# Kernel optimization log

Hardware: AMD Instinct MI355X
Metric: run time of the kernel (lower is better)

Reference implementation:

```python
import jax, jax.numpy as jnp
import numpy as np

EPS = 1e-5

def _ln(x, g, b):
    m = jnp.mean(x, axis=-1, keepdims=True)
    v = jnp.var(x, axis=-1, keepdims=True)
    return (x - m) * jax.lax.rsqrt(v + EPS) * g + b

def setup_inputs() -> dict:
    key = jax.random.key(0)
    ks = jax.random.split(key, 8)
    B, N, C, H = 2, 2048, 128, 8
    hid = 768
    s = lambda k, shp, fan: jax.random.normal(k, shp, jnp.float32) * (1.0 / np.sqrt(fan))
    return {
        "x1": jax.random.normal(ks[0], (B, N, C), jnp.float32),
        "x2": jax.random.normal(ks[1], (B, N, C), jnp.float32),
        "x3": jax.random.normal(ks[2], (B, N, C), jnp.float32),
        "ln1_g": jnp.ones((3, C), jnp.float32),
        "ln1_b": jnp.zeros((3, C), jnp.float32),
        "qkv_w": s(ks[3], (3, C, 3 * C), C),      # [branch, in, out]; torch Linear weight transposed
        "proj_w": s(ks[4], (3, C, C), C),
        "proj_b": jnp.zeros((3, C), jnp.float32),
        "ln2_g": jnp.ones((3 * C,), jnp.float32),
        "ln2_b": jnp.zeros((3 * C,), jnp.float32),
        "fc1_w": s(ks[5], (3 * C, hid), 3 * C),
        "fc1_b": jnp.zeros((hid,), jnp.float32),
        "fc2_w": s(ks[6], (hid, 3 * C), hid),
        "fc2_b": jnp.zeros((3 * C,), jnp.float32),
    }

def _branch(x, g, b, w_qkv, w_p, b_p, num_heads=8):
    B, N, C = x.shape
    hd = C // num_heads
    scale = hd ** -0.5
    xn = _ln(x, g, b)
    qkv = (xn @ w_qkv).reshape(B, N, 3, num_heads, hd)
    qkv = jnp.transpose(qkv, (2, 0, 3, 1, 4))  # [3,B,H,N,hd]
    q, k, v = qkv[0], qkv[1], qkv[2]
    attn = jax.nn.softmax(jnp.einsum('bhnd,bhmd->bhnm', q, k) * scale, axis=-1)
    o = jnp.einsum('bhnm,bhmd->bhnd', attn, v)
    o = jnp.transpose(o, (0, 2, 1, 3)).reshape(B, N, C)
    return x + (o @ w_p + b_p)

def reference(x1, x2, x3, ln1_g, ln1_b, qkv_w, proj_w, proj_b,
              ln2_g, ln2_b, fc1_w, fc1_b, fc2_w, fc2_b):
    xs = jnp.stack([x1, x2, x3])  # [3,B,N,C]
    xs = jax.vmap(_branch)(xs, ln1_g, ln1_b, qkv_w, proj_w, proj_b)
    B, N, C = x1.shape
    xc = jnp.transpose(xs, (1, 2, 0, 3)).reshape(B, N, 3 * C)  # concat(x1,x2,x3) on features
    h = jax.nn.gelu(_ln(xc, ln2_g, ln2_b) @ fc1_w + fc1_b, approximate=False)
    xc = xc + (h @ fc2_w + fc2_b)
    return xc[:, :, :C], xc[:, :, C:2 * C], xc[:, :, 2 * C:]
```

## Files before the change

### kernel.cpp

```cpp
#include <hip/hip_runtime.h>
#include <hip/hip_bf16.h>

typedef __hip_bfloat16 bf16;


static __device__ __forceinline__ float b2f(bf16 h) { return __bfloat162float(h); }
static __device__ __forceinline__ bf16 f2b(float f) { return __float2bfloat16(f); }
static __device__ __forceinline__ unsigned short f2bu(float f) {
    bf16 h = f2b(f);
    return *reinterpret_cast<unsigned short*>(&h);
}

typedef __attribute__((ext_vector_type(8))) short short8;
typedef __attribute__((ext_vector_type(4))) short short4v;
typedef __attribute__((ext_vector_type(16))) float f32x16;
typedef __attribute__((ext_vector_type(2))) int int2v;

#define QSCALE 0.36067376022224085f

static __device__ __forceinline__ float xhalf(float x, int hi) {
    auto r = __builtin_amdgcn_permlane32_swap(__float_as_int(x), __float_as_int(x), false, false);
    return __int_as_float(hi ? r[0] : r[1]);
}

__global__ __launch_bounds__(256) void k_wt_all(const float* __restrict__ qkv_w, const float* __restrict__ proj_w,
                                                const float* __restrict__ fc1_w, const float* __restrict__ fc2_w,
                                                bf16* __restrict__ wtq, bf16* __restrict__ wtp,
                                                bf16* __restrict__ wt1, bf16* __restrict__ wt2) {
    int idx = blockIdx.x * 256 + threadIdx.x;
    if (idx < 147456) {
        int b = idx / 49152, i2 = idx % 49152;
        int n = i2 >> 7, k = i2 & 127;
        wtq[idx] = f2b(qkv_w[b * 49152 + k * 384 + n]);
    } else if (idx < 196608) {
        int j = idx - 147456;
        int b = j / 16384, i2 = j % 16384;
        int n = i2 >> 7, k = i2 & 127;
        wtp[j] = f2b(proj_w[b * 16384 + k * 128 + n]);
    } else if (idx < 491520) {
        int j = idx - 196608;
        int n = j / 384, k = j - n * 384;
        wt1[j] = f2b(fc1_w[k * 768 + n]);
    } else {
        int j = idx - 491520;
        int n = j / 768, k = j - n * 768;
        wt2[j] = f2b(fc2_w[k * 384 + n]);
    }
}

__device__ __forceinline__ f32x16 gemm_tile(const short* __restrict__ A, const short* __restrict__ W,
                                            int K, int rowbase, int colbase,
                                            short* als, short* wls) {
    int tid = threadIdx.x;
    int wid = tid >> 6, lane = tid & 63;
    int hi = lane >> 5, l31 = lane & 31;
    int wm = wid >> 1, wn = wid & 1;
    int sr = tid >> 3, skb = tid & 7;
    f32x16 acc;
#pragma unroll
    for (int i = 0; i < 16; ++i) acc[i] = 0.f;
    for (int k0 = 0; k0 < K; k0 += 64) {
        __syncthreads();
#pragma unroll
        for (int pass = 0; pass < 2; ++pass) {
            int r = sr + pass * 32;
            short8 av = *(const short8*)&A[(size_t)(rowbase + r) * K + k0 + skb * 8];
            *(short8*)&als[r * 64 + ((skb ^ (r & 7)) * 8)] = av;
            short8 wv = *(const short8*)&W[(size_t)(colbase + r) * K + k0 + skb * 8];
            *(short8*)&wls[r * 64 + ((skb ^ (r & 7)) * 8)] = wv;
        }
        __syncthreads();
#pragma unroll
        for (int ks = 0; ks < 4; ++ks) {
            int ra = wm * 32 + l31;
            int rb = wn * 32 + l31;
            int kb = ks * 2 + hi;
            short8 af = *(const short8*)&als[ra * 64 + ((kb ^ (ra & 7)) * 8)];
            short8 bf = *(const short8*)&wls[rb * 64 + ((kb ^ (rb & 7)) * 8)];
            acc = __builtin_amdgcn_mfma_f32_32x32x16_bf16(af, bf, acc, 0, 0, 0);
        }
    }
    return acc;
}

__global__ __launch_bounds__(256) void k_ln1(const float* __restrict__ x1, const float* __restrict__ x2,
                                             const float* __restrict__ x3, const float* __restrict__ g,
                                             const float* __restrict__ b, bf16* __restrict__ xn) {
    int tid = threadIdx.x;
    int wave = tid >> 6, lane = tid & 63;
    int grow = blockIdx.x * 4 + wave;
    int branch = grow >> 12;
    const float* xp = (branch == 0) ? x1 : (branch == 1 ? x2 : x3);
    const float* row = xp + (size_t)(grow & 4095) * 128;
    float2 a = *reinterpret_cast<const float2*>(&row[2 * lane]);
    float s = a.x + a.y, sq = a.x * a.x + a.y * a.y;
#pragma unroll
    for (int off = 32; off >= 1; off >>= 1) { s += __shfl_xor(s, off); sq += __shfl_xor(sq, off); }
    float mean = s * (1.f / 128.f);
    float var = sq * (1.f / 128.f) - mean * mean;
    float rstd = rsqrtf(var + 1e-5f);
    float2 gv = *reinterpret_cast<const float2*>(&g[branch * 128 + 2 * lane]);
    float2 bv = *reinterpret_cast<const float2*>(&b[branch * 128 + 2 * lane]);
    bf16* orow = xn + (size_t)grow * 128;
    orow[2 * lane] = f2b((a.x - mean) * rstd * gv.x + bv.x);
    orow[2 * lane + 1] = f2b((a.y - mean) * rstd * gv.y + bv.y);
}

__global__ __launch_bounds__(256) void k_qkv_m(const bf16* __restrict__ xn, const bf16* __restrict__ wt,
                                               bf16* __restrict__ q, bf16* __restrict__ k, bf16* __restrict__ v) {
    __shared__ short als[64 * 64];
    __shared__ short wls[64 * 64];
    int branch = blockIdx.z;
    const short* A = (const short*)xn + (size_t)branch * 4096 * 128;
    const short* W = (const short*)wt + (size_t)branch * 384 * 128;
    int rowbase = blockIdx.x * 64, colbase = blockIdx.y * 64;
    f32x16 acc = gemm_tile(A, W, 128, rowbase, colbase, als, wls);
    int tid = threadIdx.x, wid = tid >> 6, lane = tid & 63;
    int hi = lane >> 5, l31 = lane & 31;
    int wm = wid >> 1, wn = wid & 1;
    int c = colbase + wn * 32 + l31;
    int which = c >> 7, h = (c >> 4) & 7, d = c & 15;
    bf16* dst = (which == 0) ? q : (which == 1 ? k : v);
    float scl = (which == 0) ? QSCALE : 1.0f;
#pragma unroll
    for (int i = 0; i < 16; ++i) {
        int mrow = (i & 3) + 8 * (i >> 2) + 4 * hi;
        int token = rowbase + wm * 32 + mrow;
        int bb = token >> 11, n = token & 2047;
        dst[((((size_t)branch * 2 + bb) * 8 + h) * 2048 + n) * 16 + d] = f2b(acc[i] * scl);
    }
}

__global__ __launch_bounds__(128, 4) void k_attn(const bf16* __restrict__ qg, const bf16* __restrict__ kg,
                                                 const bf16* __restrict__ vg, bf16* __restrict__ o) {
    __shared__ short vt[2][16 * 64];
    int bh = blockIdx.x;
    int qblk = blockIdx.y;
    size_t base = (size_t)bh * (2048 * 16);
    int tid = threadIdx.x, wave = tid >> 6, lane = tid & 63;
    int hi = lane >> 5, l31 = lane & 31;
    int qrow = qblk * 64 + wave * 32 + l31;
    const short* qs = (const short*)qg;
    const short* ks = (const short*)kg;
    const short* vs = (const short*)vg;
    short8 qf = *(const short8*)&qs[base + (size_t)qrow * 16 + hi * 8];

    f32x16 acc;
    f32x16 negm;
#pragma unroll
    for (int r = 0; r < 16; ++r) { acc[r] = 0.f; negm[r] = -16.f; }
    float m = 16.f, sum = 0.f;

    int sd = tid & 15, sk0 = (tid >> 4) * 8;
    int swzs = (sd & 7) << 3;

    {
        short va[8];
#pragma unroll
        for (int j = 0; j < 8; ++j) va[j] = vs[base + (size_t)(sk0 + j) * 16 + sd];
        short8 wv;
#pragma unroll
        for (int j = 0; j < 8; ++j) wv[j] = va[j];
        *(short8*)&vt[0][sd * 64 + (sk0 ^ swzs)] = wv;
    }
    __syncthreads();

    for (int c0 = 0; c0 < 2048; c0 += 64) {
        int cur = (c0 >> 6) & 1;
        bool more = (c0 + 64) < 2048;
        short8 kf0 = *(const short8*)&ks[base + (size_t)(c0 + l31) * 16 + hi * 8];
        short8 kf1 = *(const short8*)&ks[base + (size_t)(c0 + 32 + l31) * 16 + hi * 8];
        short va[8];
        if (more) {
#pragma unroll
            for (int j = 0; j < 8; ++j) va[j] = vs[base + (size_t)(c0 + 64 + sk0 + j) * 16 + sd];
        }
        f32x16 pa = __builtin_amdgcn_mfma_f32_32x32x16_bf16(kf0, qf, negm, 0, 0, 0);
        f32x16 pb = __builtin_amdgcn_mfma_f32_32x32x16_bf16(kf1, qf, negm, 0, 0, 0);
#pragma unroll
        for (int r = 0; r < 16; ++r) pa[r] = __builtin_amdgcn_exp2f(pa[r]);
#pragma unroll
        for (int r = 0; r < 16; ++r) pb[r] = __builtin_amdgcn_exp2f(pb[r]);
        float e0 = 0.f, e1 = 0.f, e2 = 0.f, e3 = 0.f;
#pragma unroll
        for (int r = 0; r < 16; r += 4) { e0 += pa[r]; e1 += pa[r + 1]; e2 += pa[r + 2]; e3 += pa[r + 3]; }
#pragma unroll
        for (int r = 0; r < 16; r += 4) { e0 += pb[r]; e1 += pb[r + 1]; e2 += pb[r + 2]; e3 += pb[r + 3]; }
        float psum = (e0 + e1) + (e2 + e3);
        if (__any(psum > 256.f)) {
            float p0 = fmaxf(pa[0], pa[1]), p1 = fmaxf(pa[2], pa[3]);
#pragma unroll
            for (int r = 4; r < 16; r += 4) { p0 = fmaxf(p0, fmaxf(pa[r], pa[r + 1])); p1 = fmaxf(p1, fmaxf(pa[r + 2], pa[r + 3])); }
#pragma unroll
            for (int r = 0; r < 16; r += 4) { p0 = fmaxf(p0, fmaxf(pb[r], pb[r + 1])); p1 = fmaxf(p1, fmaxf(pb[r + 2], pb[r + 3])); }
            float pmax = fmaxf(p0, p1);
            pmax = fmaxf(pmax, xhalf(pmax, hi));
            float delta = fmaxf(0.f, __log2f(pmax));
            float fac = __builtin_amdgcn_exp2f(-delta);
            m += delta;
#pragma unroll
            for (int r = 0; r < 16; ++r) negm[r] = -m;
            sum *= fac; psum *= fac;
#pragma unroll
            for (int r = 0; r < 16; ++r) { pa[r] *= fac; pb[r] *= fac; acc[r] *= fac; }
        }
        sum += psum;
        unsigned wa[8], wb[8];
#pragma unroll
        for (int e = 0; e < 8; ++e) {
            unsigned t;
            asm("v_cvt_pk_bf16_f32 %0, %1, %2" : "=v"(t) : "v"(pa[2 * e]), "v"(pa[2 * e + 1]));
            wa[e] = t;
            asm("v_cvt_pk_bf16_f32 %0, %1, %2" : "=v"(t) : "v"(pb[2 * e]), "v"(pb[2 * e + 1]));
            wb[e] = t;
        }
        union { unsigned u[4]; short8 v; } b1, b2, b3, b4;
        {
            auto r0 = __builtin_amdgcn_permlane32_swap((int)wa[0], (int)wa[2], false, false);
            b1.u[0] = (unsigned)r0[0]; b1.u[2] = (unsigned)r0[1];
            auto r1 = __builtin_amdgcn_permlane32_swap((int)wa[1], (int)wa[3], false, false);
            b1.u[1] = (unsigned)r1[0]; b1.u[3] = (unsigned)r1[1];
            auto r2 = __builtin_amdgcn_permlane32_swap((int)wa[4], (int)wa[6], false, false);
            b2.u[0] = (unsigned)r2[0]; b2.u[2] = (unsigned)r2[1];
            auto r3 = __builtin_amdgcn_permlane32_swap((int)wa[5], (int)wa[7], false, false);
            b2.u[1] = (unsigned)r3[0]; b2.u[3] = (unsigned)r3[1];
            auto r4 = __builtin_amdgcn_permlane32_swap((int)wb[0], (int)wb[2], false, false);
            b3.u[0] = (unsigned)r4[0]; b3.u[2] = (unsigned)r4[1];
            auto r5 = __builtin_amdgcn_permlane32_swap((int)wb[1], (int)wb[3], false, false);
            b3.u[1] = (unsigned)r5[0]; b3.u[3] = (unsigned)r5[1];
            auto r6 = __builtin_amdgcn_permlane32_swap((int)wb[4], (int)wb[6], false, false);
            b4.u[0] = (unsigned)r6[0]; b4.u[2] = (unsigned)r6[1];
            auto r7 = __builtin_amdgcn_permlane32_swap((int)wb[5], (int)wb[7], false, false);
            b4.u[1] = (unsigned)r7[0]; b4.u[3] = (unsigned)r7[1];
        }
        int d = lane & 15;
        short8 vf;
        vf = *(const short8*)&vt[cur][(d * 64 + hi * 8) ^ ((d & 7) << 3)];
        acc = __builtin_amdgcn_mfma_f32_32x32x16_bf16(vf, b1.v, acc, 0, 0, 0);
        vf = *(const short8*)&vt[cur][(d * 64 + 16 + hi * 8) ^ ((d & 7) << 3)];
        acc = __builtin_amdgcn_mfma_f32_32x32x16_bf16(vf, b2.v, acc, 0, 0, 0);
        vf = *(const short8*)&vt[cur][(d * 64 + 32 + hi * 8) ^ ((d & 7) << 3)];
        acc = __builtin_amdgcn_mfma_f32_32x32x16_bf16(vf, b3.v, acc, 0, 0, 0);
        vf = *(const short8*)&vt[cur][(d * 64 + 48 + hi * 8) ^ ((d & 7) << 3)];
        acc = __builtin_amdgcn_mfma_f32_32x32x16_bf16(vf, b4.v, acc, 0, 0, 0);
        if (more) {
            short8 wv;
#pragma unroll
            for (int j = 0; j < 8; ++j) wv[j] = va[j];
            *(short8*)&vt[cur ^ 1][sd * 64 + (sk0 ^ swzs)] = wv;
        }
        __syncthreads();
    }
    sum += xhalf(sum, hi);
    float inv = 1.f / sum;
    int branch = bh >> 4, bb = (bh >> 3) & 1, h = bh & 7;
    size_t orow = (size_t)branch * 4096 + (size_t)bb * 2048 + qrow;
    unsigned u0 = (unsigned)f2bu(acc[0] * inv) | ((unsigned)f2bu(acc[1] * inv) << 16);
    unsigned u1 = (unsigned)f2bu(acc[2] * inv) | ((unsigned)f2bu(acc[3] * inv) << 16);
    unsigned u2 = (unsigned)f2bu(acc[4] * inv) | ((unsigned)f2bu(acc[5] * inv) << 16);
    unsigned u3 = (unsigned)f2bu(acc[6] * inv) | ((unsigned)f2bu(acc[7] * inv) << 16);
    short* op = (short*)o;
    int2v w01; w01.x = (int)u0; w01.y = (int)u1;
    int2v w23; w23.x = (int)u2; w23.y = (int)u3;
    *(int2v*)&op[orow * 128 + h * 16 + 4 * hi] = w01;
    *(int2v*)&op[orow * 128 + h * 16 + 8 + 4 * hi] = w23;
}

__global__ __launch_bounds__(256) void k_proj_m(const bf16* __restrict__ ob, const bf16* __restrict__ wt,
                                                const float* __restrict__ pb, const float* __restrict__ x1,
                                                const float* __restrict__ x2, const float* __restrict__ x3,
                                                float* __restrict__ xc) {
    __shared__ short als[64 * 64];
    __shared__ short wls[64 * 64];
    int branch = blockIdx.z;
    const short* A = (const short*)ob + (size_t)branch * 4096 * 128;
    const short* W = (const short*)wt + (size_t)branch * 128 * 128;
    int rowbase = blockIdx.x * 64, colbase = blockIdx.y * 64;
    f32x16 acc = gemm_tile(A, W, 128, rowbase, colbase, als, wls);
    int tid = threadIdx.x, wid = tid >> 6, lane = tid & 63;
    int hi = lane >> 5, l31 = lane & 31;
    int wm = wid >> 1, wn = wid & 1;
    int c = colbase + wn * 32 + l31;
    float bias = pb[branch * 128 + c];
    const float* xp = (branch == 0) ? x1 : (branch == 1 ? x2 : x3);
#pragma unroll
    for (int i = 0; i < 16; ++i) {
        int mrow = (i & 3) + 8 * (i >> 2) + 4 * hi;
        int row = rowbase + wm * 32 + mrow;
        xc[(size_t)row * 384 + branch * 128 + c] = acc[i] + bias + xp[(size_t)row * 128 + c];
    }
}

__global__ __launch_bounds__(256) void k_ln2(const float* __restrict__ xc, const float* __restrict__ g,
                                             const float* __restrict__ b, bf16* __restrict__ xcn) {
    int tid = threadIdx.x, wave = tid >> 6, lane = tid & 63;
    int row = blockIdx.x * 4 + wave;
    const float* rp = xc + (size_t)row * 384;
    float v[6];
    float s = 0.f, sq = 0.f;
#pragma unroll
    for (int i = 0; i < 6; ++i) {
        v[i] = rp[lane + i * 64];
        s += v[i]; sq += v[i] * v[i];
    }
#pragma unroll
    for (int off = 32; off >= 1; off >>= 1) { s += __shfl_xor(s, off); sq += __shfl_xor(sq, off); }
    float mean = s * (1.f / 384.f);
    float var = sq * (1.f / 384.f) - mean * mean;
    float rstd = rsqrtf(var + 1e-5f);
    bf16* op = xcn + (size_t)row * 384;
#pragma unroll
    for (int i = 0; i < 6; ++i) {
        int c = lane + i * 64;
        op[c] = f2b((v[i] - mean) * rstd * g[c] + b[c]);
    }
}

__global__ __launch_bounds__(256) void k_fc1_m(const bf16* __restrict__ xcn, const bf16* __restrict__ wt,
                                               const float* __restrict__ bias, bf16* __restrict__ h) {
    __shared__ short als[64 * 64];
    __shared__ short wls[64 * 64];
    const short* A = (const short*)xcn;
    const short* W = (const short*)wt;
    int rowbase = blockIdx.x * 64, colbase = blockIdx.y * 64;
    f32x16 acc = gemm_tile(A, W, 384, rowbase, colbase, als, wls);
    int tid = threadIdx.x, wid = tid >> 6, lane = tid & 63;
    int hi = lane >> 5, l31 = lane & 31;
    int wm = wid >> 1, wn = wid & 1;
    int c = colbase + wn * 32 + l31;
    float bs = bias[c];
#pragma unroll
    for (int i = 0; i < 16; ++i) {
        int mrow = (i & 3) + 8 * (i >> 2) + 4 * hi;
        int row = rowbase + wm * 32 + mrow;
        float vv = acc[i] + bs;
        float ge = 0.5f * vv * (1.f + erff(vv * 0.70710678118f));
        h[(size_t)row * 768 + c] = f2b(ge);
    }
}

__global__ __launch_bounds__(256) void k_fc2_m(const bf16* __restrict__ h, const bf16* __restrict__ wt,
                                               const float* __restrict__ bias, const float* __restrict__ xc,
                                               float* __restrict__ outp) {
    __shared__ short als[64 * 64];
    __shared__ short wls[64 * 64];
    const short* A = (const short*)h;
    const short* W = (const short*)wt;
    int rowbase = blockIdx.x * 64, colbase = blockIdx.y * 64;
    f32x16 acc = gemm_tile(A, W, 768, rowbase, colbase, als, wls);
    int tid = threadIdx.x, wid = tid >> 6, lane = tid & 63;
    int hi = lane >> 5, l31 = lane & 31;
    int wm = wid >> 1, wn = wid & 1;
    int c = colbase + wn * 32 + l31;
    float bs = bias[c];
    int which = c >> 7, cc = c & 127;
#pragma unroll
    for (int i = 0; i < 16; ++i) {
        int mrow = (i & 3) + 8 * (i >> 2) + 4 * hi;
        int row = rowbase + wm * 32 + mrow;
        outp[(size_t)which * 524288 + (size_t)row * 128 + cc] = acc[i] + bs + xc[(size_t)row * 384 + c];
    }
}

extern "C" void kernel_launch(void* const* d_in, const int* in_sizes, int n_in,
                              void* d_out, int out_size, void* d_ws, size_t ws_size,
                              hipStream_t stream) {
    const float* x1     = (const float*)d_in[0];
    const float* x2     = (const float*)d_in[1];
    const float* x3     = (const float*)d_in[2];
    const float* ln1_g  = (const float*)d_in[3];
    const float* ln1_b  = (const float*)d_in[4];
    const float* qkv_w  = (const float*)d_in[5];
    const float* proj_w = (const float*)d_in[6];
    const float* proj_b = (const float*)d_in[7];
    const float* ln2_g  = (const float*)d_in[8];
    const float* ln2_b  = (const float*)d_in[9];
    const float* fc1_w  = (const float*)d_in[10];
    const float* fc1_b  = (const float*)d_in[11];
    const float* fc2_w  = (const float*)d_in[12];
    const float* fc2_b  = (const float*)d_in[13];

    char* ws = (char*)d_ws;
    const size_t SB = 3145728;
    bf16* xn  = (bf16*)(ws + 0 * SB);
    bf16* qb  = (bf16*)(ws + 1 * SB);
    bf16* kb  = (bf16*)(ws + 2 * SB);
    bf16* vb  = (bf16*)(ws + 3 * SB);
    bf16* ob  = (bf16*)(ws + 4 * SB);
    float* xc = (float*)(ws + 5 * SB);
    bf16* xcn = (bf16*)(ws + 5 * SB + 6291456);
    bf16* hb  = (bf16*)(ws + 6 * SB + 6291456);
    char* wbase = ws + 31457280;
    bf16* wtq = (bf16*)(wbase);
    bf16* wtp = (bf16*)(wbase + 294912);
    bf16* wt1 = (bf16*)(wbase + 393216);
    bf16* wt2 = (bf16*)(wbase + 983040);

    k_wt_all<<<3072, 256, 0, stream>>>(qkv_w, proj_w, fc1_w, fc2_w, wtq, wtp, wt1, wt2);
    k_ln1<<<3072, 256, 0, stream>>>(x1, x2, x3, ln1_g, ln1_b, xn);
    k_qkv_m<<<dim3(64, 6, 3), 256, 0, stream>>>(xn, wtq, qb, kb, vb);
    k_attn<<<dim3(48, 32), 128, 0, stream>>>(qb, kb, vb, ob);
    k_proj_m<<<dim3(64, 2, 3), 256, 0, stream>>>(ob, wtp, proj_b, x1, x2, x3, xc);
    k_ln2<<<1024, 256, 0, stream>>>(xc, ln2_g, ln2_b, xcn);
    k_fc1_m<<<dim3(64, 12, 1), 256, 0, stream>>>(xcn, wt1, fc1_b, hb);
    k_fc2_m<<<dim3(64, 6, 1), 256, 0, stream>>>(hb, wt2, fc2_b, xc, (float*)d_out);
}
```

Measured before the change: 103.2 us.

## Split attention over two key halves with a separate log-sum-exp reduction kernel

Attention is split along the key dimension into two halves (grid z=2), doubling the number of blocks. Each block writes unnormalized bf16 partial outputs plus a row sum and max. A new reduction kernel rescales and combines the two partials and normalizes them into the output. This targets low occupancy from only 1536 blocks of 128 threads. In exchange it adds a kernel launch, extra global traffic for the partials, and extra bf16 rounding of the unnormalized accumulators.

```diff
diff --git a/kernel.cpp b/kernel.cpp
--- a/kernel.cpp
+++ b/kernel.cpp
@@ -9,6 +9,9 @@
 static __device__ __forceinline__ unsigned short f2bu(float f) {
     bf16 h = f2b(f);
     return *reinterpret_cast<unsigned short*>(&h);
+}
+static __device__ __forceinline__ float bs2f(short s) {
+    return __uint_as_float(((unsigned)(unsigned short)s) << 16);
 }
 
 typedef __attribute__((ext_vector_type(8))) short short8;
@@ -132,10 +135,12 @@
 }
 
 __global__ __launch_bounds__(128, 4) void k_attn(const bf16* __restrict__ qg, const bf16* __restrict__ kg,
-                                                 const bf16* __restrict__ vg, bf16* __restrict__ o) {
+                                                 const bf16* __restrict__ vg, bf16* __restrict__ pacc,
+                                                 float2* __restrict__ psm) {
     __shared__ short vt[2][16 * 64];
     int bh = blockIdx.x;
     int qblk = blockIdx.y;
+    int split = blockIdx.z;
     size_t base = (size_t)bh * (2048 * 16);
     int tid = threadIdx.x, wave = tid >> 6, lane = tid & 63;
     int hi = lane >> 5, l31 = lane & 31;
@@ -153,11 +158,12 @@
 
     int sd = tid & 15, sk0 = (tid >> 4) * 8;
     int swzs = (sd & 7) << 3;
+    int kbeg = split * 1024, kend = kbeg + 1024;
 
     {
         short va[8];
 #pragma unroll
-        for (int j = 0; j < 8; ++j) va[j] = vs[base + (size_t)(sk0 + j) * 16 + sd];
+        for (int j = 0; j < 8; ++j) va[j] = vs[base + (size_t)(kbeg + sk0 + j) * 16 + sd];
         short8 wv;
 #pragma unroll
         for (int j = 0; j < 8; ++j) wv[j] = va[j];
@@ -165,9 +171,9 @@
     }
     __syncthreads();
 
-    for (int c0 = 0; c0 < 2048; c0 += 64) {
+    for (int c0 = kbeg; c0 < kend; c0 += 64) {
         int cur = (c0 >> 6) & 1;
-        bool more = (c0 + 64) < 2048;
+        bool more = (c0 + 64) < kend;
         short8 kf0 = *(const short8*)&ks[base + (size_t)(c0 + l31) * 16 + hi * 8];
         short8 kf1 = *(const short8*)&ks[base + (size_t)(c0 + 32 + l31) * 16 + hi * 8];
         short va[8];
@@ -251,14 +257,60 @@
         }
         __syncthreads();
     }
-    sum += xhalf(sum, hi);
-    float inv = 1.f / sum;
+    float sumt = sum + xhalf(sum, hi);
+    size_t pidx = ((size_t)(split * 48 + bh) * 2048 + qrow) * 16;
+    unsigned u0 = (unsigned)f2bu(acc[0]) | ((unsigned)f2bu(acc[1]) << 16);
+    unsigned u1 = (unsigned)f2bu(acc[2]) | ((unsigned)f2bu(acc[3]) << 16);
+    unsigned u2 = (unsigned)f2bu(acc[4]) | ((unsigned)f2bu(acc[5]) << 16);
+    unsigned u3 = (unsigned)f2bu(acc[6]) | ((unsigned)f2bu(acc[7]) << 16);
+    short* pp = (short*)pacc;
+    int2v w01; w01.x = (int)u0; w01.y = (int)u1;
+    int2v w23; w23.x = (int)u2; w23.y = (int)u3;
+    *(int2v*)&pp[pidx + 4 * hi] = w01;
+    *(int2v*)&pp[pidx + 8 + 4 * hi] = w23;
+    if (hi == 0) {
+        float2 sm; sm.x = sumt; sm.y = m;
+        psm[(size_t)(split * 48 + bh) * 2048 + qrow] = sm;
+    }
+}
+
+__global__ __launch_bounds__(256) void k_attn_red(const bf16* __restrict__ pacc, const float2* __restrict__ psm,
+                                                  bf16* __restrict__ o) {
+    int t = blockIdx.x * 256 + threadIdx.x;
+    int hi = t & 1;
+    int qrow = (t >> 1) & 2047;
+    int bh = t >> 12;
+    size_t ridx = (size_t)bh * 2048 + qrow;
+    float2 sm0 = psm[ridx];
+    float2 sm1 = psm[(size_t)48 * 2048 + ridx];
+    float mp = fmaxf(sm0.y, sm1.y);
+    float w0 = __builtin_amdgcn_exp2f(sm0.y - mp);
+    float w1 = __builtin_amdgcn_exp2f(sm1.y - mp);
+    float inv = 1.f / (sm0.x * w0 + sm1.x * w1);
+    w0 *= inv; w1 *= inv;
+    const short* p0 = (const short*)pacc + ridx * 16;
+    const short* p1 = (const short*)pacc + (size_t)48 * 2048 * 16 + ridx * 16;
+    short4v a0 = *(const short4v*)&p0[4 * hi];
+    short4v c0 = *(const short4v*)&p0[8 + 4 * hi];
+    short4v a1 = *(const short4v*)&p1[4 * hi];
+    short4v c1 = *(const short4v*)&p1[8 + 4 * hi];
+    unsigned u0, u1, u2, u3;
+    {
+        float f0 = bs2f(a0[0]) * w0 + bs2f(a1[0]) * w1;
+        float f1 = bs2f(a0[1]) * w0 + bs2f(a1[1]) * w1;
+        float f2 = bs2f(a0[2]) * w0 + bs2f(a1[2]) * w1;
+        float f3 = bs2f(a0[3]) * w0 + bs2f(a1[3]) * w1;
+        u0 = (unsigned)f2bu(f0) | ((unsigned)f2bu(f1) << 16);
+        u1 = (unsigned)f2bu(f2) | ((unsigned)f2bu(f3) << 16);
+        float g0 = bs2f(c0[0]) * w0 + bs2f(c1[0]) * w1;
+        float g1 = bs2f(c0[1]) * w0 + bs2f(c1[1]) * w1;
+        float g2 = bs2f(c0[2]) * w0 + bs2f(c1[2]) * w1;
+        float g3 = bs2f(c0[3]) * w0 + bs2f(c1[3]) * w1;
+        u2 = (unsigned)f2bu(g0) | ((unsigned)f2bu(g1) << 16);
+        u3 = (unsigned)f2bu(g2) | ((unsigned)f2bu(g3) << 16);
+    }
     int branch = bh >> 4, bb = (bh >> 3) & 1, h = bh & 7;
     size_t orow = (size_t)branch * 4096 + (size_t)bb * 2048 + qrow;
-    unsigned u0 = (unsigned)f2bu(acc[0] * inv) | ((unsigned)f2bu(acc[1] * inv) << 16);
-    unsigned u1 = (unsigned)f2bu(acc[2] * inv) | ((unsigned)f2bu(acc[3] * inv) << 16);
-    unsigned u2 = (unsigned)f2bu(acc[4] * inv) | ((unsigned)f2bu(acc[5] * inv) << 16);
-    unsigned u3 = (unsigned)f2bu(acc[6] * inv) | ((unsigned)f2bu(acc[7] * inv) << 16);
     short* op = (short*)o;
     int2v w01; w01.x = (int)u0; w01.y = (int)u1;
     int2v w23; w23.x = (int)u2; w23.y = (int)u3;
@@ -395,11 +447,14 @@
     bf16* wtp = (bf16*)(wbase + 294912);
     bf16* wt1 = (bf16*)(wbase + 393216);
     bf16* wt2 = (bf16*)(wbase + 983040);
+    bf16*  pacc = (bf16*)(ws + 22020096);
+    float2* psm = (float2*)(ws + 28311552);
 
     k_wt_all<<<3072, 256, 0, stream>>>(qkv_w, proj_w, fc1_w, fc2_w, wtq, wtp, wt1, wt2);
     k_ln1<<<3072, 256, 0, stream>>>(x1, x2, x3, ln1_g, ln1_b, xn);
     k_qkv_m<<<dim3(64, 6, 3), 256, 0, stream>>>(xn, wtq, qb, kb, vb);
-    k_attn<<<dim3(48, 32), 128, 0, stream>>>(qb, kb, vb, ob);
+    k_attn<<<dim3(48, 32, 2), 128, 0, stream>>>(qb, kb, vb, pacc, psm);
+    k_attn_red<<<768, 256, 0, stream>>>(pacc, psm, ob);
     k_proj_m<<<dim3(64, 2, 3), 256, 0, stream>>>(ob, wtp, proj_b, x1, x2, x3, xc);
     k_ln2<<<1024, 256, 0, stream>>>(xc, ln2_g, ln2_b, xcn);
     k_fc1_m<<<dim3(64, 12, 1), 256, 0, stream>>>(xcn, wt1, fc1_b, hb);
```

After: 104.4 us. About the same (+1.2%).
